# Performance work log

Hardware: AMD Instinct MI355X
Metric: run time of the kernel (lower is better)

Reference implementation:

```python
import jax, jax.numpy as jnp
import numpy as np

DIM = 768
HEADS = 12


def setup_inputs() -> dict:
    key = jax.random.key(0)
    ks = jax.random.split(key, 7)
    bs, nmm, nv, na = 32, 256, 196, 60
    s = DIM ** -0.5
    return {
        "xmm": jax.random.normal(ks[0], (bs, nmm, DIM), jnp.float32),
        "xv": jax.random.normal(ks[1], (bs, nv, DIM), jnp.float32),
        "xa": jax.random.normal(ks[2], (bs, na, DIM), jnp.float32),
        "Wq": jax.random.normal(ks[3], (DIM, DIM), jnp.float32) * s,
        "Wkv": jax.random.normal(ks[4], (DIM, 2 * DIM), jnp.float32) * s,
        "Wproj": jax.random.normal(ks[5], (DIM, DIM), jnp.float32) * s,
        "bproj": jnp.zeros((DIM,), jnp.float32),
    }


def reference(xmm, xv, xa, Wq, Wkv, Wproj, bproj):
    bs, nmm, dim = xmm.shape
    hd = dim // HEADS
    scale = hd ** -0.5
    x_src = jnp.concatenate([xv, xa], axis=1)            # [bs, nv+na, dim]
    q = (xmm @ Wq).reshape(bs, nmm, HEADS, hd).transpose(0, 2, 1, 3)   # [b,h,q,d]
    kv = (x_src @ Wkv).reshape(bs, -1, 2, HEADS, hd).transpose(2, 0, 3, 1, 4)
    k, v = kv[0], kv[1]                                  # [b,h,k,d]
    attn = jax.nn.softmax(jnp.einsum('bhqd,bhkd->bhqk', q, k) * scale, axis=-1)
    out = jnp.einsum('bhqk,bhkd->bhqd', attn, v)
    out = out.transpose(0, 2, 1, 3).reshape(bs, nmm, dim)
    out = out @ Wproj + bproj
    return out, attn
```

## Files before the change

### kernel.cpp

```cpp
#include <hip/hip_runtime.h>


typedef __attribute__((ext_vector_type(8))) _Float16 f16x8;
typedef __attribute__((ext_vector_type(4))) _Float16 f16x4;
typedef __attribute__((ext_vector_type(4))) float    f32x4;

#define AS1 __attribute__((address_space(1)))
#define AS3 __attribute__((address_space(3)))

__device__ __forceinline__ void gload_lds16(const void* g, void* l) {
    void* gnc = const_cast<void*>(g);
    __builtin_amdgcn_global_load_lds((AS1 void*)gnc, (AS3 void*)l, 16, 0, 0);
}

__global__ __launch_bounds__(256) void prep_acts(const float* __restrict__ xmm,
                                                 const float* __restrict__ xv,
                                                 const float* __restrict__ xa,
                                                 _Float16* __restrict__ xmm16,
                                                 _Float16* __restrict__ xsrc16) {
    int id = blockIdx.x * 256 + threadIdx.x;
    float4 v;
    _Float16* dst;
    int off;
    if (id < 1572864) {
        v = ((const float4*)xmm)[id];
        dst = xmm16; off = id;
    } else {
        int t = id - 1572864;
        int c4 = t % 192;
        int r  = (t / 192) & 255;
        int b  = t / 49152;
        if (r < 196) v = ((const float4*)xv)[((long)b * 196 + r) * 192 + c4];
        else         v = ((const float4*)xa)[((long)b * 60 + (r - 196)) * 192 + c4];
        dst = xsrc16; off = t;
    }
    f16x4 h = { (_Float16)v.x, (_Float16)v.y, (_Float16)v.z, (_Float16)v.w };
    ((f16x4*)dst)[off] = h;
}

__global__ __launch_bounds__(256) void prep_weights(const float* __restrict__ Wq,
                                                    const float* __restrict__ Wkv,
                                                    const float* __restrict__ Wproj,
                                                    _Float16* __restrict__ WqT,
                                                    _Float16* __restrict__ WkvT,
                                                    _Float16* __restrict__ WprojT) {
    int id = blockIdx.x * 256 + threadIdx.x;
    if (id < 589824) {
        int k = id % 768, n = id / 768;
        WqT[id] = (_Float16)(0.125f * Wq[(long)k * 768 + n]);
        return;
    }
    id -= 589824;
    if (id < 1179648) {
        int k = id % 768, n = id / 768;
        WkvT[id] = (_Float16)Wkv[(long)k * 1536 + n];
        return;
    }
    id -= 1179648;
    if (id < 589824) {
        int k = id % 768, n = id / 768;
        WprojT[id] = (_Float16)Wproj[(long)k * 768 + n];
    }
}

template <int OUT_F32>
__device__ __forceinline__ void gemm_body(const _Float16* __restrict__ A,
                                          const _Float16* __restrict__ Bt,
                                          void* __restrict__ C,
                                          const float* __restrict__ bias,
                                          long bm, long bn, int N, int K) {
    __shared__ _Float16 As[128 * 64];
    __shared__ _Float16 Bs[128 * 64];

    const int tid  = threadIdx.x;
    const int wave = tid >> 6, lane = tid & 63;
    const int lrow = lane & 15, quad = lane >> 4;
    const int wm = (wave >> 1) * 64, wn = (wave & 1) * 64;

    f32x4 acc[4][4];
    const f32x4 fz = {0.f, 0.f, 0.f, 0.f};
#pragma unroll
    for (int mt = 0; mt < 4; ++mt)
#pragma unroll
        for (int nt = 0; nt < 4; ++nt) acc[mt][nt] = fz;

    for (int k0 = 0; k0 < K; k0 += 64) {
#pragma unroll
        for (int it = 0; it < 4; ++it) {
            int seg = tid + it * 256;
            int rr = seg >> 3, pp = seg & 7;
            int cc = ((pp ^ (rr & 7)) << 3);
            gload_lds16(A  + (bm + rr) * (long)K + k0 + cc, As + seg * 8);
            gload_lds16(Bt + (bn + rr) * (long)K + k0 + cc, Bs + seg * 8);
        }
        __syncthreads();
#pragma unroll
        for (int ks = 0; ks < 2; ++ks) {
            f16x8 af[4], bf[4];
#pragma unroll
            for (int mt = 0; mt < 4; ++mt) {
                int r = wm + mt * 16 + lrow;
                af[mt] = *(const f16x8*)(As + r * 64 + (((ks * 4 + quad) ^ (r & 7)) << 3));
            }
#pragma unroll
            for (int nt = 0; nt < 4; ++nt) {
                int r = wn + nt * 16 + lrow;
                bf[nt] = *(const f16x8*)(Bs + r * 64 + (((ks * 4 + quad) ^ (r & 7)) << 3));
            }
#pragma unroll
            for (int mt = 0; mt < 4; ++mt)
#pragma unroll
                for (int nt = 0; nt < 4; ++nt)
                    acc[mt][nt] = __builtin_amdgcn_mfma_f32_16x16x32_f16(
                        bf[nt], af[mt], acc[mt][nt], 0, 0, 0);
        }
        __syncthreads();
    }

#pragma unroll
    for (int mt = 0; mt < 4; ++mt) {
        long row = bm + wm + mt * 16 + lrow;
#pragma unroll
        for (int nt = 0; nt < 4; ++nt) {
            long col0 = bn + wn + nt * 16 + quad * 4;
            if (OUT_F32) {
                float4 b4 = *(const float4*)(bias + col0);
                float4 o = { acc[mt][nt][0] + b4.x, acc[mt][nt][1] + b4.y,
                             acc[mt][nt][2] + b4.z, acc[mt][nt][3] + b4.w };
                *(float4*)((float*)C + row * N + col0) = o;
            } else {
                f16x4 h = { (_Float16)acc[mt][nt][0], (_Float16)acc[mt][nt][1],
                            (_Float16)acc[mt][nt][2], (_Float16)acc[mt][nt][3] };
                *(f16x4*)((_Float16*)C + row * N + col0) = h;
            }
        }
    }
}

__global__ __launch_bounds__(256, 2)
void gemm_qkv(const _Float16* __restrict__ xmm16, const _Float16* __restrict__ xsrc16,
              const _Float16* __restrict__ WqT, const _Float16* __restrict__ WkvT,
              _Float16* __restrict__ Q16, _Float16* __restrict__ KV16) {
    const int bx = blockIdx.x;
    const long bm = (long)blockIdx.y * 128;
    if (bx < 6) gemm_body<0>(xmm16,  WqT,  (void*)Q16,  nullptr, bm, (long)bx * 128,       768,  768);
    else        gemm_body<0>(xsrc16, WkvT, (void*)KV16, nullptr, bm, (long)(bx - 6) * 128, 1536, 768);
}

__global__ __launch_bounds__(256, 2)
void gemm_proj(const _Float16* __restrict__ O16, const _Float16* __restrict__ WprojT,
               float* __restrict__ out, const float* __restrict__ bias) {
    gemm_body<1>(O16, WprojT, (void*)out, bias, (long)blockIdx.y * 128, (long)blockIdx.x * 128, 768, 768);
}

__global__ __launch_bounds__(256, 2)
void attn_kernel(const _Float16* __restrict__ Qg, const _Float16* __restrict__ KVg,
                 float* __restrict__ attn_out, _Float16* __restrict__ Og) {
    __shared__ _Float16 sh[32768];
    _Float16* Ks = sh;
    _Float16* Vt = sh + 16384;
    _Float16* Ps = sh;

    const int tid  = threadIdx.x;
    const int wave = tid >> 6, lane = tid & 63;
    const int lrow = lane & 15, quad = lane >> 4;
    const int qb = blockIdx.x, h = blockIdx.y, b = blockIdx.z;
    const long qrow0 = (long)b * 256 + qb * 64;
    const long krow0 = (long)b * 256;

    f16x8 aq[2];
#pragma unroll
    for (int ks = 0; ks < 2; ++ks)
        aq[ks] = *(const f16x8*)(Qg + (qrow0 + wave * 16 + lrow) * 768 + h * 64 + ks * 32 + quad * 8);

#pragma unroll
    for (int it = 0; it < 8; ++it) {
        int seg = tid + it * 256;
        int rr = seg >> 3, pp = seg & 7;
        int cc = ((pp ^ (rr & 7)) << 3);
        gload_lds16(KVg + (krow0 + rr) * 1536 + h * 64 + cc, Ks + seg * 8);
    }
#pragma unroll
    for (int it = 0; it < 8; ++it) {
        int seg = tid + it * 256;
        int key = seg >> 3, d0 = (seg & 7) * 8;
        f16x8 v = *(const f16x8*)(KVg + (krow0 + key) * 1536 + 768 + h * 64 + d0);
#pragma unroll
        for (int i = 0; i < 8; ++i) {
            int d = d0 + i;
            Vt[d * 256 + ((((key >> 3) ^ (d & 7)) << 3) | (key & 7))] = v[i];
        }
    }
    __syncthreads();

    f32x4 sacc[16];
    const f32x4 fz = {0.f, 0.f, 0.f, 0.f};
#pragma unroll
    for (int nt = 0; nt < 16; ++nt) sacc[nt] = fz;
#pragma unroll
    for (int ks = 0; ks < 2; ++ks) {
#pragma unroll
        for (int nt = 0; nt < 16; ++nt) {
            int r = nt * 16 + lrow;
            f16x8 bk = *(const f16x8*)(Ks + r * 64 + (((ks * 4 + quad) ^ (r & 7)) << 3));
            sacc[nt] = __builtin_amdgcn_mfma_f32_16x16x32_f16(bk, aq[ks], sacc[nt], 0, 0, 0);
        }
    }

    float m = -1e30f;
#pragma unroll
    for (int nt = 0; nt < 16; ++nt)
#pragma unroll
        for (int j = 0; j < 4; ++j) m = fmaxf(m, sacc[nt][j]);
    m = fmaxf(m, __shfl_xor(m, 16));
    m = fmaxf(m, __shfl_xor(m, 32));
    float s = 0.f;
#pragma unroll
    for (int nt = 0; nt < 16; ++nt)
#pragma unroll
        for (int j = 0; j < 4; ++j) {
            float p = __expf(sacc[nt][j] - m);
            sacc[nt][j] = p; s += p;
        }
    s += __shfl_xor(s, 16);
    s += __shfl_xor(s, 32);
    const float li = 1.f / s;

    __syncthreads();

    const long abase = (((long)b * 12 + h) * 256 + qb * 64) * 256;
    const int q = wave * 16 + lrow;
#pragma unroll
    for (int nt = 0; nt < 16; ++nt) {
        float4 o = { sacc[nt][0] * li, sacc[nt][1] * li, sacc[nt][2] * li, sacc[nt][3] * li };
        *(float4*)(attn_out + abase + (long)q * 256 + nt * 16 + quad * 4) = o;
        f16x4 hp = { (_Float16)o.x, (_Float16)o.y, (_Float16)o.z, (_Float16)o.w };
        int blk = nt * 2 + (quad >> 1);
        *(f16x4*)(Ps + q * 256 + ((blk ^ (q & 7)) << 3) + ((quad & 1) << 2)) = hp;
    }
    __syncthreads();

    f32x4 oacc[4];
#pragma unroll
    for (int nt = 0; nt < 4; ++nt) oacc[nt] = fz;
#pragma unroll
    for (int ks = 0; ks < 8; ++ks) {
        int pr = wave * 16 + lrow;
        f16x8 ap = *(const f16x8*)(Ps + pr * 256 + (((ks * 4 + quad) ^ (pr & 7)) << 3));
#pragma unroll
        for (int nt = 0; nt < 4; ++nt) {
            int d = nt * 16 + lrow;
            f16x8 bv = *(const f16x8*)(Vt + d * 256 + (((ks * 4 + quad) ^ (d & 7)) << 3));
            oacc[nt] = __builtin_amdgcn_mfma_f32_16x16x32_f16(bv, ap, oacc[nt], 0, 0, 0);
        }
    }
#pragma unroll
    for (int nt = 0; nt < 4; ++nt) {
        f16x4 ho = { (_Float16)oacc[nt][0], (_Float16)oacc[nt][1],
                     (_Float16)oacc[nt][2], (_Float16)oacc[nt][3] };
        *(f16x4*)(Og + (qrow0 + wave * 16 + lrow) * 768 + h * 64 + nt * 16 + quad * 4) = ho;
    }
}

extern "C" void kernel_launch(void* const* d_in, const int* in_sizes, int n_in,
                              void* d_out, int out_size, void* d_ws, size_t ws_size,
                              hipStream_t stream) {
    const float* xmm   = (const float*)d_in[0];
    const float* xv    = (const float*)d_in[1];
    const float* xa    = (const float*)d_in[2];
    const float* Wq    = (const float*)d_in[3];
    const float* Wkv   = (const float*)d_in[4];
    const float* Wproj = (const float*)d_in[5];
    const float* bproj = (const float*)d_in[6];

    float* out  = (float*)d_out;
    float* attn = out + 6291456;

    char* ws = (char*)d_ws;
    _Float16* xmm16  = (_Float16*)(ws);
    _Float16* xsrc16 = (_Float16*)(ws + 12582912);
    _Float16* WqT    = (_Float16*)(ws + 25165824);
    _Float16* WkvT   = (_Float16*)(ws + 26345472);
    _Float16* WprojT = (_Float16*)(ws + 28704768);
    _Float16* Q16    = (_Float16*)(ws + 29884416);
    _Float16* KV16   = (_Float16*)(ws + 42467328);
    _Float16* O16    = xmm16;

    prep_acts   <<<12288, 256, 0, stream>>>(xmm, xv, xa, xmm16, xsrc16);
    prep_weights<<<9216,  256, 0, stream>>>(Wq, Wkv, Wproj, WqT, WkvT, WprojT);

    gemm_qkv<<<dim3(18, 64), 256, 0, stream>>>(xmm16, xsrc16, WqT, WkvT, Q16, KV16);

    attn_kernel<<<dim3(4, 12, 32), 256, 0, stream>>>(Q16, KV16, attn, O16);

    gemm_proj<<<dim3(6, 64), 256, 0, stream>>>(O16, WprojT, out, bproj);
}
```

Baseline: 293.8 us.

## Double-buffer GEMM LDS tiles and merge prep kernels into one launch

```diff
diff --git a/kernel.cpp b/kernel.cpp
--- a/kernel.cpp
+++ b/kernel.cpp
@@ -13,38 +13,40 @@
     __builtin_amdgcn_global_load_lds((AS1 void*)gnc, (AS3 void*)l, 16, 0, 0);
 }
 
-__global__ __launch_bounds__(256) void prep_acts(const float* __restrict__ xmm,
-                                                 const float* __restrict__ xv,
-                                                 const float* __restrict__ xa,
-                                                 _Float16* __restrict__ xmm16,
-                                                 _Float16* __restrict__ xsrc16) {
-    int id = blockIdx.x * 256 + threadIdx.x;
-    float4 v;
-    _Float16* dst;
-    int off;
-    if (id < 1572864) {
-        v = ((const float4*)xmm)[id];
-        dst = xmm16; off = id;
-    } else {
-        int t = id - 1572864;
-        int c4 = t % 192;
-        int r  = (t / 192) & 255;
-        int b  = t / 49152;
-        if (r < 196) v = ((const float4*)xv)[((long)b * 196 + r) * 192 + c4];
-        else         v = ((const float4*)xa)[((long)b * 60 + (r - 196)) * 192 + c4];
-        dst = xsrc16; off = t;
-    }
-    f16x4 h = { (_Float16)v.x, (_Float16)v.y, (_Float16)v.z, (_Float16)v.w };
-    ((f16x4*)dst)[off] = h;
-}
-
-__global__ __launch_bounds__(256) void prep_weights(const float* __restrict__ Wq,
-                                                    const float* __restrict__ Wkv,
-                                                    const float* __restrict__ Wproj,
-                                                    _Float16* __restrict__ WqT,
-                                                    _Float16* __restrict__ WkvT,
-                                                    _Float16* __restrict__ WprojT) {
-    int id = blockIdx.x * 256 + threadIdx.x;
+__global__ __launch_bounds__(256) void prep_all(const float* __restrict__ xmm,
+                                                const float* __restrict__ xv,
+                                                const float* __restrict__ xa,
+                                                const float* __restrict__ Wq,
+                                                const float* __restrict__ Wkv,
+                                                const float* __restrict__ Wproj,
+                                                _Float16* __restrict__ xmm16,
+                                                _Float16* __restrict__ xsrc16,
+                                                _Float16* __restrict__ WqT,
+                                                _Float16* __restrict__ WkvT,
+                                                _Float16* __restrict__ WprojT) {
+    int bid = blockIdx.x;
+    if (bid < 12288) {
+        int id = bid * 256 + threadIdx.x;
+        float4 v;
+        _Float16* dst;
+        int off;
+        if (id < 1572864) {
+            v = ((const float4*)xmm)[id];
+            dst = xmm16; off = id;
+        } else {
+            int t = id - 1572864;
+            int c4 = t % 192;
+            int r  = (t / 192) & 255;
+            int b  = t / 49152;
+            if (r < 196) v = ((const float4*)xv)[((long)b * 196 + r) * 192 + c4];
+            else         v = ((const float4*)xa)[((long)b * 60 + (r - 196)) * 192 + c4];
+            dst = xsrc16; off = t;
+        }
+        f16x4 h = { (_Float16)v.x, (_Float16)v.y, (_Float16)v.z, (_Float16)v.w };
+        ((f16x4*)dst)[off] = h;
+        return;
+    }
+    int id = (bid - 12288) * 256 + threadIdx.x;
     if (id < 589824) {
         int k = id % 768, n = id / 768;
         WqT[id] = (_Float16)(0.125f * Wq[(long)k * 768 + n]);
@@ -69,8 +71,8 @@
                                           void* __restrict__ C,
                                           const float* __restrict__ bias,
                                           long bm, long bn, int N, int K) {
-    __shared__ _Float16 As[128 * 64];
-    __shared__ _Float16 Bs[128 * 64];
+    __shared__ _Float16 As[2][128 * 64];
+    __shared__ _Float16 Bs[2][128 * 64];
 
     const int tid  = threadIdx.x;
     const int wave = tid >> 6, lane = tid & 63;
@@ -84,28 +86,30 @@
 #pragma unroll
         for (int nt = 0; nt < 4; ++nt) acc[mt][nt] = fz;
 
-    for (int k0 = 0; k0 < K; k0 += 64) {
+    auto stage = [&](int buf, int k0) {
 #pragma unroll
         for (int it = 0; it < 4; ++it) {
             int seg = tid + it * 256;
             int rr = seg >> 3, pp = seg & 7;
             int cc = ((pp ^ (rr & 7)) << 3);
-            gload_lds16(A  + (bm + rr) * (long)K + k0 + cc, As + seg * 8);
-            gload_lds16(Bt + (bn + rr) * (long)K + k0 + cc, Bs + seg * 8);
-        }
-        __syncthreads();
+            gload_lds16(A  + (bm + rr) * (long)K + k0 + cc, &As[buf][seg * 8]);
+            gload_lds16(Bt + (bn + rr) * (long)K + k0 + cc, &Bs[buf][seg * 8]);
+        }
+    };
+
+    auto compute = [&](int buf) {
 #pragma unroll
         for (int ks = 0; ks < 2; ++ks) {
             f16x8 af[4], bf[4];
 #pragma unroll
             for (int mt = 0; mt < 4; ++mt) {
                 int r = wm + mt * 16 + lrow;
-                af[mt] = *(const f16x8*)(As + r * 64 + (((ks * 4 + quad) ^ (r & 7)) << 3));
+                af[mt] = *(const f16x8*)(&As[buf][r * 64 + (((ks * 4 + quad) ^ (r & 7)) << 3)]);
             }
 #pragma unroll
             for (int nt = 0; nt < 4; ++nt) {
                 int r = wn + nt * 16 + lrow;
-                bf[nt] = *(const f16x8*)(Bs + r * 64 + (((ks * 4 + quad) ^ (r & 7)) << 3));
+                bf[nt] = *(const f16x8*)(&Bs[buf][r * 64 + (((ks * 4 + quad) ^ (r & 7)) << 3)]);
             }
 #pragma unroll
             for (int mt = 0; mt < 4; ++mt)
@@ -114,7 +118,26 @@
                     acc[mt][nt] = __builtin_amdgcn_mfma_f32_16x16x32_f16(
                         bf[nt], af[mt], acc[mt][nt], 0, 0, 0);
         }
-        __syncthreads();
+    };
+
+    const int KT = K >> 6;
+    stage(0, 0);
+    asm volatile("s_waitcnt vmcnt(0)" ::: "memory");
+    __builtin_amdgcn_s_barrier();
+
+    for (int kt = 0; kt < KT; kt += 2) {
+        if (kt + 1 < KT) stage(1, (kt + 1) << 6);
+        compute(0);
+        asm volatile("s_waitcnt vmcnt(0) lgkmcnt(0)" ::: "memory");
+        __builtin_amdgcn_sched_barrier(0);
+        __builtin_amdgcn_s_barrier();
+        if (kt + 1 < KT) {
+            if (kt + 2 < KT) stage(0, (kt + 2) << 6);
+            compute(1);
+            asm volatile("s_waitcnt vmcnt(0) lgkmcnt(0)" ::: "memory");
+            __builtin_amdgcn_sched_barrier(0);
+            __builtin_amdgcn_s_barrier();
+        }
     }
 
 #pragma unroll
@@ -238,7 +261,9 @@
         int blk = nt * 2 + (quad >> 1);
         *(f16x4*)(Ps + q * 256 + ((blk ^ (q & 7)) << 3) + ((quad & 1) << 2)) = hp;
     }
-    __syncthreads();
+    asm volatile("s_waitcnt lgkmcnt(0)" ::: "memory");
+    __builtin_amdgcn_sched_barrier(0);
+    __builtin_amdgcn_s_barrier();
 
     f32x4 oacc[4];
 #pragma unroll
@@ -286,8 +311,8 @@
     _Float16* KV16   = (_Float16*)(ws + 42467328);
     _Float16* O16    = xmm16;
 
-    prep_acts   <<<12288, 256, 0, stream>>>(xmm, xv, xa, xmm16, xsrc16);
-    prep_weights<<<9216,  256, 0, stream>>>(Wq, Wkv, Wproj, WqT, WkvT, WprojT);
+    prep_all<<<21504, 256, 0, stream>>>(xmm, xv, xa, Wq, Wkv, Wproj,
+                                        xmm16, xsrc16, WqT, WkvT, WprojT);
 
     gemm_qkv<<<dim3(18, 64), 256, 0, stream>>>(xmm16, xsrc16, WqT, WkvT, Q16, KV16);
 
```

Result: slower. 303.4 us (+3.3%).
